# Kernel optimization log

Hardware: AMD Instinct MI355X
Metric: run time of the kernel (lower is better)

The kernel has to match this reference:

```python
import jax, jax.numpy as jnp
import numpy as np
import math

SAMPLING_FACTOR = 5


def setup_inputs() -> dict:
    key = jax.random.key(0)
    kq, kk, kv, ki = jax.random.split(key, 4)
    B, L_Q, L_K, d = 8, 4096, 4096, 64
    # U_part = min(5 * L_Q * ceil(log1p(L_K)), L_K) = 4096 for these sizes
    U_part = min(SAMPLING_FACTOR * L_Q * math.ceil(math.log1p(L_K)), L_K)
    q = jax.random.normal(kq, (B, L_Q, d), dtype=jnp.float32)
    K = jax.random.normal(kk, (B, L_K, d), dtype=jnp.float32)
    V = jax.random.normal(kv, (B, L_K, d), dtype=jnp.float32)
    index_sample = jax.random.randint(ki, (U_part,), 0, L_K)  # random key sample (torch.randint)
    return {"q": q, "K": K, "V": V, "index_sample": index_sample}


def reference(q, K, V, index_sample):
    B, L_Q, d = q.shape
    L_K = K.shape[1]
    log_L_Q = math.ceil(math.log1p(L_Q))
    u = min(SAMPLING_FACTOR * log_L_Q, L_Q)  # number of selected queries (45 here)

    # Random key sampling (indices shared across batch)
    K_sample = K[:, index_sample, :]                       # [B, U_part, d]
    # Q @ K_sample^T
    Q_K_sample = jnp.einsum('bqd,bud->bqu', q, K_sample)   # [B, L_Q, U_part]
    # Sparsity measure M = max - sum/L_K
    M = Q_K_sample.max(axis=-1) - Q_K_sample.sum(axis=-1) / L_K  # [B, L_Q]
    # Source uses topk(..., largest=False): pick queries with SMALLEST M (kept faithfully)
    _, M_top = jax.lax.top_k(-M, u)                        # [B, u]
    # Gather the selected queries
    Q_reduce = jnp.take_along_axis(q, M_top[:, :, None], axis=1)  # [B, u, d]
    # Full attention over all keys for the selected queries
    attn_scores = jnp.einsum('bud,bkd->buk', Q_reduce, K) / math.sqrt(d)  # [B, u, L_K]
    attn_probs = jax.nn.softmax(attn_scores, axis=-1)
    attn_output = jnp.einsum('buk,bkd->bud', attn_probs, V)  # [B, u, d]
    return attn_output, attn_scores
```

## Files before the change

### kernel.cpp

```cpp
#include <hip/hip_runtime.h>
#include <hip/hip_bf16.h>
#include <math.h>

#define BB 8
#define LQ 4096
#define LK 4096
#define DD 64
#define UU 45
#define CCAP 256
#define CUMTHR 96
#define ECH 32
#define PCH 32
#define MCG 4

typedef __bf16 bf16x8 __attribute__((ext_vector_type(8)));
typedef unsigned short ushort8 __attribute__((ext_vector_type(8)));
typedef float f32x4 __attribute__((ext_vector_type(4)));

__device__ inline unsigned short f2bf(float x) {
    unsigned u = __builtin_bit_cast(unsigned, x);
    return (unsigned short)((u + 0x7FFF + ((u >> 16) & 1)) >> 16);
}

__device__ inline void gl_lds16(const void* g, void* l) {
    __builtin_amdgcn_global_load_lds(
        (const __attribute__((address_space(1))) unsigned int*)g,
        (__attribute__((address_space(3))) unsigned int*)l, 16, 0, 0);
}

__global__ __launch_bounds__(256) void k_gatherK(const float* __restrict__ K,
                                                 const int* __restrict__ idx,
                                                 int Upart,
                                                 unsigned short* __restrict__ Kg,
                                                 double* __restrict__ part) {
    int b = blockIdx.y;
    int chunk = blockIdx.x;
    int u0 = chunk * 256;
    int t = threadIdx.x;
    int pt = t & 7;

    double acc[8] = {0,0,0,0,0,0,0,0};
    #pragma unroll
    for (int i = 0; i < 8; ++i) {
        int lin = i * 256 + t;
        int u = u0 + (lin >> 3);
        if (u < Upart) {
            int kr = idx[u];
            const float* src = &K[((size_t)b * LK + kr) * DD + pt * 8];
            float4 v0 = *(const float4*)src;
            float4 v1 = *(const float4*)(src + 4);
            ushort8 pk;
            pk[0]=f2bf(v0.x); pk[1]=f2bf(v0.y); pk[2]=f2bf(v0.z); pk[3]=f2bf(v0.w);
            pk[4]=f2bf(v1.x); pk[5]=f2bf(v1.y); pk[6]=f2bf(v1.z); pk[7]=f2bf(v1.w);
            *(ushort8*)&Kg[((size_t)b * 4096 + u) * 64 + pt * 8] = pk;
            acc[0] += (double)v0.x; acc[1] += (double)v0.y;
            acc[2] += (double)v0.z; acc[3] += (double)v0.w;
            acc[4] += (double)v1.x; acc[5] += (double)v1.y;
            acc[6] += (double)v1.z; acc[7] += (double)v1.w;
        }
    }
    __shared__ double sred[32][64];
    int rg = t >> 3;
    #pragma unroll
    for (int j = 0; j < 8; ++j) sred[rg][pt * 8 + j] = acc[j];
    __syncthreads();
    if (t < 64) {
        double s = 0.0;
        #pragma unroll
        for (int r = 0; r < 32; ++r) s += sred[r][t];
        part[((size_t)(b * 16 + chunk)) * 64 + t] = s;
    }
}

__global__ __launch_bounds__(256) void k_mfmaM(const float* __restrict__ Q,
                                               const unsigned short* __restrict__ Kg,
                                               float* __restrict__ maxpart) {
    int bx = blockIdx.x, cg = blockIdx.y, b = blockIdx.z;
    int t = threadIdx.x;
    int lane = t & 63, w = t >> 6;
    int row0 = bx * 256;

    __shared__ unsigned short Qs[256 * 64];
    __shared__ unsigned short Ks[2][128 * 64];

    for (int i = 0; i < 8; ++i) {
        int u = i * 256 + t;
        int r = u >> 3, s = u & 7;
        int c = s ^ (r & 7);
        const float* src = &Q[((size_t)b * LQ + row0 + r) * DD + c * 8];
        float4 v0 = *(const float4*)src;
        float4 v1 = *(const float4*)(src + 4);
        ushort8 pk;
        pk[0]=f2bf(v0.x); pk[1]=f2bf(v0.y); pk[2]=f2bf(v0.z); pk[3]=f2bf(v0.w);
        pk[4]=f2bf(v1.x); pk[5]=f2bf(v1.y); pk[6]=f2bf(v1.z); pk[7]=f2bf(v1.w);
        *(ushort8*)&Qs[r * 64 + s * 8] = pk;
    }

    int krl = lane >> 3;
    int kc8 = (lane & 7) ^ (krl & 7);
    const unsigned short* kgb = Kg + ((size_t)b * 4096 + cg * 1024) * 64;

    #define STAGE_K(buf, tile)                                                  \
        {                                                                       \
            _Pragma("unroll")                                                   \
            for (int i_ = 0; i_ < 4; ++i_) {                                    \
                int seg_ = w * 4 + i_;                                          \
                const unsigned short* g_ =                                      \
                    kgb + ((size_t)((tile) * 128 + seg_ * 8 + krl)) * 64 + kc8 * 8; \
                gl_lds16(g_, &Ks[buf][seg_ * 512]);                             \
            }                                                                   \
        }

    STAGE_K(0, 0)
    __syncthreads();

    bf16x8 afr[4][2];
    #pragma unroll
    for (int rf = 0; rf < 4; ++rf)
        #pragma unroll
        for (int kh = 0; kh < 2; ++kh) {
            int r = w * 64 + rf * 16 + (lane & 15);
            int slot = (kh * 4 + (lane >> 4)) ^ (r & 7);
            afr[rf][kh] = __builtin_bit_cast(bf16x8, *(const ushort8*)&Qs[r * 64 + slot * 8]);
        }

    float rowmax[4][4];
    #pragma unroll
    for (int rf = 0; rf < 4; ++rf)
        #pragma unroll
        for (int g = 0; g < 4; ++g) rowmax[rf][g] = -INFINITY;

    for (int tile = 0; tile < 8; ++tile) {
        int cur = tile & 1;
        if (tile < 7) STAGE_K(cur ^ 1, tile + 1)

        #pragma unroll
        for (int cf = 0; cf < 8; ++cf) {
            f32x4 acc[4];
            #pragma unroll
            for (int rf = 0; rf < 4; ++rf) acc[rf] = (f32x4){0.f, 0.f, 0.f, 0.f};
            #pragma unroll
            for (int kh = 0; kh < 2; ++kh) {
                int ccol = cf * 16 + (lane & 15);
                int slot = (kh * 4 + (lane >> 4)) ^ (ccol & 7);
                bf16x8 bfr = __builtin_bit_cast(bf16x8, *(const ushort8*)&Ks[cur][ccol * 64 + slot * 8]);
                #pragma unroll
                for (int rf = 0; rf < 4; ++rf)
                    acc[rf] = __builtin_amdgcn_mfma_f32_16x16x32_bf16(afr[rf][kh], bfr, acc[rf], 0, 0, 0);
            }
            #pragma unroll
            for (int rf = 0; rf < 4; ++rf)
                #pragma unroll
                for (int g = 0; g < 4; ++g)
                    rowmax[rf][g] = fmaxf(rowmax[rf][g], acc[rf][g]);
        }
        __syncthreads();
    }

    #pragma unroll
    for (int rf = 0; rf < 4; ++rf)
        #pragma unroll
        for (int g = 0; g < 4; ++g) {
            float m = rowmax[rf][g];
            m = fmaxf(m, __shfl_xor(m, 1));
            m = fmaxf(m, __shfl_xor(m, 2));
            m = fmaxf(m, __shfl_xor(m, 4));
            m = fmaxf(m, __shfl_xor(m, 8));
            if ((lane & 15) == 0) {
                int row = row0 + w * 64 + rf * 16 + (lane >> 4) * 4 + g;
                maxpart[((size_t)(b * MCG + cg)) * LQ + row] = m;
            }
        }
}

__global__ __launch_bounds__(256) void k_meanmerge(const float* __restrict__ Q,
                                                   const double* __restrict__ part,
                                                   int nch,
                                                   const float* __restrict__ maxpart,
                                                   double* __restrict__ mt,
                                                   float* __restrict__ Map) {
    int b = blockIdx.y;
    int t = threadIdx.x;
    int r = blockIdx.x * 256 + t;
    __shared__ double sK[64];
    if (t < 64) {
        double s = 0.0;
        for (int ch = 0; ch < nch; ++ch)
            s += part[((size_t)(b * 16 + ch)) * 64 + t];
        sK[t] = s;
    }
    __syncthreads();
    const float* qr = &Q[((size_t)b * LQ + r) * DD];
    double a0 = 0, a1 = 0, a2 = 0, a3 = 0;
    #pragma unroll
    for (int d = 0; d < 64; d += 4) {
        a0 += (double)qr[d + 0] * sK[d + 0];
        a1 += (double)qr[d + 1] * sK[d + 1];
        a2 += (double)qr[d + 2] * sK[d + 2];
        a3 += (double)qr[d + 3] * sK[d + 3];
    }
    double m = ((a0 + a1) + (a2 + a3)) / (double)LK;
    mt[(size_t)b * LQ + r] = m;
    float mx = fmaxf(fmaxf(maxpart[((size_t)(b * MCG + 0)) * LQ + r],
                           maxpart[((size_t)(b * MCG + 1)) * LQ + r]),
                     fmaxf(maxpart[((size_t)(b * MCG + 2)) * LQ + r],
                           maxpart[((size_t)(b * MCG + 3)) * LQ + r]));
    Map[(size_t)b * LQ + r] = mx - (float)m;
}

__global__ __launch_bounds__(256) void k_select(const float* __restrict__ Map,
                                                int* __restrict__ cand,
                                                int* __restrict__ cand_count) {
    int b = blockIdx.x;
    int t = threadIdx.x;
    __shared__ float mv[LQ];
    __shared__ int hist[1024];
    __shared__ int seg[256];
    __shared__ float wmin[4], wmax[4];
    __shared__ float s_min, s_max;
    __shared__ int s_bstar, s_cnt;

    float lmin = INFINITY, lmax = -INFINITY;
    for (int i = t; i < LQ; i += 256) {
        float v = Map[(size_t)b * LQ + i];
        mv[i] = v;
        lmin = fminf(lmin, v);
        lmax = fmaxf(lmax, v);
    }
    #pragma unroll
    for (int m = 1; m < 64; m <<= 1) {
        lmin = fminf(lmin, __shfl_xor(lmin, m));
        lmax = fmaxf(lmax, __shfl_xor(lmax, m));
    }
    int wid = t >> 6;
    if ((t & 63) == 0) { wmin[wid] = lmin; wmax[wid] = lmax; }
    for (int i = t; i < 1024; i += 256) hist[i] = 0;
    __syncthreads();
    if (t == 0) {
        s_min = fminf(fminf(wmin[0], wmin[1]), fminf(wmin[2], wmin[3]));
        s_max = fmaxf(fmaxf(wmax[0], wmax[1]), fmaxf(wmax[2], wmax[3]));
        s_cnt = 0;
        s_bstar = 1023;
    }
    __syncthreads();
    float vmin = s_min;
    float w = (s_max - vmin) * (1.0f / 1024.0f);
    if (w <= 0.f) w = 1e-30f;
    float inv = 1.0f / w;
    for (int i = t; i < LQ; i += 256) {
        int bin = (int)((mv[i] - vmin) * inv);
        bin = min(max(bin, 0), 1023);
        atomicAdd(&hist[bin], 1);
    }
    __syncthreads();
    int h0 = hist[t * 4 + 0], h1 = hist[t * 4 + 1];
    int h2 = hist[t * 4 + 2], h3 = hist[t * 4 + 3];
    seg[t] = h0 + h1 + h2 + h3;
    __syncthreads();
    for (int off = 1; off < 256; off <<= 1) {
        int v = seg[t];
        int add = (t >= off) ? seg[t - off] : 0;
        __syncthreads();
        seg[t] = v + add;
        __syncthreads();
    }
    {
        int prev = (t == 0) ? 0 : seg[t - 1];
        if (seg[t] >= CUMTHR && prev < CUMTHR) {
            int cum = prev, bs = t * 4 + 3;
            if (cum + h0 >= CUMTHR) bs = t * 4;
            else if (cum + h0 + h1 >= CUMTHR) bs = t * 4 + 1;
            else if (cum + h0 + h1 + h2 >= CUMTHR) bs = t * 4 + 2;
            s_bstar = bs;
        }
    }
    __syncthreads();
    int bstar = s_bstar;
    for (int i = t; i < LQ; i += 256) {
        int bin = (int)((mv[i] - vmin) * inv);
        bin = min(max(bin, 0), 1023);
        if (bin <= bstar) {
            int p = atomicAdd(&s_cnt, 1);
            if (p < CCAP) cand[b * CCAP + p] = i;
        }
    }
    __syncthreads();
    if (t == 0) cand_count[b] = min(s_cnt, CCAP);
}

__global__ __launch_bounds__(256, 1) void k_exact(const float* __restrict__ Q,
                                                  const float* __restrict__ K,
                                                  const int* __restrict__ idx,
                                                  const int* __restrict__ cand,
                                                  const int* __restrict__ cand_count,
                                                  float* __restrict__ exactpart) {
    int kc = blockIdx.x;
    int b  = blockIdx.y;
    int t = threadIdx.x;
    int lane = t & 63, w = t >> 6;
    __shared__ float Ks[128 * 64];
    __shared__ float wmx[4][CCAP];

    #pragma unroll
    for (int p = 0; p < 8; ++p) {
        int row = p * 16 + (t >> 4);
        int c4 = t & 15;
        int kr = idx[kc * 128 + row];
        *(float4*)&Ks[row * 64 + c4 * 4] =
            *(const float4*)&K[((size_t)b * LK + kr) * DD + c4 * 4];
    }

    int count = cand_count[b];
    int npass = (count + 127) >> 7;
    __syncthreads();

    for (int pass = 0; pass < npass; ++pass) {
        int s0 = pass * 128 + lane;
        int s1 = s0 + 64;
        float4 q0[16], q1[16];
        {
            float4 z = {0.f, 0.f, 0.f, 0.f};
            if (s0 < count) {
                const float4* qp = (const float4*)&Q[((size_t)b * LQ + cand[b * CCAP + s0]) * DD];
                #pragma unroll
                for (int i = 0; i < 16; ++i) q0[i] = qp[i];
            } else {
                #pragma unroll
                for (int i = 0; i < 16; ++i) q0[i] = z;
            }
            if (s1 < count) {
                const float4* qp = (const float4*)&Q[((size_t)b * LQ + cand[b * CCAP + s1]) * DD];
                #pragma unroll
                for (int i = 0; i < 16; ++i) q1[i] = qp[i];
            } else {
                #pragma unroll
                for (int i = 0; i < 16; ++i) q1[i] = z;
            }
        }

        float m0 = -INFINITY, m1 = -INFINITY;
        int kbeg = w * 32;
        for (int k = kbeg; k < kbeg + 32; ++k) {
            const float4* kr4 = (const float4*)&Ks[k * 64];
            float a0=0.f,a1=0.f,a2=0.f,a3=0.f;
            float c0=0.f,c1=0.f,c2=0.f,c3=0.f;
            #pragma unroll
            for (int i = 0; i < 16; i += 4) {
                float4 kv0 = kr4[i+0], kv1 = kr4[i+1], kv2 = kr4[i+2], kv3 = kr4[i+3];
                a0 = fmaf(q0[i+0].x, kv0.x, a0); a0 = fmaf(q0[i+0].y, kv0.y, a0);
                a0 = fmaf(q0[i+0].z, kv0.z, a0); a0 = fmaf(q0[i+0].w, kv0.w, a0);
                a1 = fmaf(q0[i+1].x, kv1.x, a1); a1 = fmaf(q0[i+1].y, kv1.y, a1);
                a1 = fmaf(q0[i+1].z, kv1.z, a1); a1 = fmaf(q0[i+1].w, kv1.w, a1);
                a2 = fmaf(q0[i+2].x, kv2.x, a2); a2 = fmaf(q0[i+2].y, kv2.y, a2);
                a2 = fmaf(q0[i+2].z, kv2.z, a2); a2 = fmaf(q0[i+2].w, kv2.w, a2);
                a3 = fmaf(q0[i+3].x, kv3.x, a3); a3 = fmaf(q0[i+3].y, kv3.y, a3);
                a3 = fmaf(q0[i+3].z, kv3.z, a3); a3 = fmaf(q0[i+3].w, kv3.w, a3);
                c0 = fmaf(q1[i+0].x, kv0.x, c0); c0 = fmaf(q1[i+0].y, kv0.y, c0);
                c0 = fmaf(q1[i+0].z, kv0.z, c0); c0 = fmaf(q1[i+0].w, kv0.w, c0);
                c1 = fmaf(q1[i+1].x, kv1.x, c1); c1 = fmaf(q1[i+1].y, kv1.y, c1);
                c1 = fmaf(q1[i+1].z, kv1.z, c1); c1 = fmaf(q1[i+1].w, kv1.w, c1);
                c2 = fmaf(q1[i+2].x, kv2.x, c2); c2 = fmaf(q1[i+2].y, kv2.y, c2);
                c2 = fmaf(q1[i+2].z, kv2.z, c2); c2 = fmaf(q1[i+2].w, kv2.w, c2);
                c3 = fmaf(q1[i+3].x, kv3.x, c3); c3 = fmaf(q1[i+3].y, kv3.y, c3);
                c3 = fmaf(q1[i+3].z, kv3.z, c3); c3 = fmaf(q1[i+3].w, kv3.w, c3);
            }
            m0 = fmaxf(m0, (a0 + a1) + (a2 + a3));
            m1 = fmaxf(m1, (c0 + c1) + (c2 + c3));
        }
        wmx[w][s0] = m0;
        if (s1 < CCAP) wmx[w][s1] = m1;
    }
    __syncthreads();

    if (t < count) {
        float m = fmaxf(fmaxf(wmx[0][t], wmx[1][t]), fmaxf(wmx[2][t], wmx[3][t]));
        exactpart[((size_t)(b * CCAP + t)) * ECH + kc] = m;
    }
}

__global__ __launch_bounds__(64) void k_final45(const float* __restrict__ exactpart,
                                                const double* __restrict__ mt,
                                                const int* __restrict__ cand,
                                                const int* __restrict__ cand_count,
                                                int* __restrict__ Mtop) {
    int b = blockIdx.x;
    int l = threadIdx.x;
    int count = cand_count[b];
    float val[4];
    int oid[4];
    #pragma unroll
    for (int j = 0; j < 4; ++j) {
        int slot = l + j * 64;
        if (slot < count) {
            const float* ep = &exactpart[((size_t)(b * CCAP + slot)) * ECH];
            float m = ep[0];
            #pragma unroll
            for (int k = 1; k < ECH; ++k) m = fmaxf(m, ep[k]);
            int r = cand[b * CCAP + slot];
            val[j] = m - (float)mt[(size_t)b * LQ + r];
            oid[j] = r;
        } else { val[j] = INFINITY; oid[j] = 0x7FFFFFFF; }
    }
    for (int it = 0; it < UU; ++it) {
        float bv = val[0]; int bi = oid[0], bj = 0;
        #pragma unroll
        for (int j = 1; j < 4; ++j)
            if (val[j] < bv || (val[j] == bv && oid[j] < bi)) { bv = val[j]; bi = oid[j]; bj = j; }
        float rv = bv; int ri = bi;
        #pragma unroll
        for (int m = 1; m < 64; m <<= 1) {
            float ov = __shfl_xor(rv, m);
            int oi = __shfl_xor(ri, m);
            if (ov < rv || (ov == rv && oi < ri)) { rv = ov; ri = oi; }
        }
        if (l == 0) Mtop[b * UU + it] = ri;
        if (rv == bv && ri == bi) val[bj] = INFINITY;
    }
}

__global__ __launch_bounds__(256) void k_spv(const float* __restrict__ Q,
                                             const float* __restrict__ K,
                                             const float* __restrict__ V,
                                             const int* __restrict__ Mtop,
                                             float* __restrict__ scores,
                                             float2* __restrict__ stats,
                                             float* __restrict__ partial) {
    int ch = blockIdx.x, b = blockIdx.y;
    int t = threadIdx.x;
    int lane = t & 63, w = t >> 6;
    int k0 = ch * 128;

    __shared__ float Qs[48][64];
    __shared__ float Vs[128 * 64];
    __shared__ float Ps[48][128];
    __shared__ float2 st[48];

    for (int i = t; i < 48 * 64; i += 256) {
        int r = i >> 6, dd = i & 63;
        Qs[r][dd] = (r < UU) ? Q[((size_t)b * LQ + Mtop[b * UU + r]) * DD + dd] : 0.f;
    }
    for (int p = 0; p < 8; ++p) {
        int lin = p * 1024 + t * 4;
        *(float4*)&Vs[lin] = *(const float4*)&V[((size_t)b * LK + k0) * DD + lin];
    }
    __syncthreads();

    {
        int key = t & 127;
        int rh = t >> 7;
        int r0 = rh * 23;
        int r1 = rh ? UU : 23;
        const float* Krow = &K[((size_t)(b * LK + k0 + key)) * DD];
        float4 kv[16];
        #pragma unroll
        for (int i = 0; i < 16; ++i) kv[i] = ((const float4*)Krow)[i];
        for (int r = r0; r < r1; ++r) {
            const float4* qr = (const float4*)&Qs[r][0];
            float d0 = 0.f, d1 = 0.f, d2 = 0.f, d3 = 0.f;
            #pragma unroll
            for (int i = 0; i < 16; i += 4) {
                float4 q0 = qr[i+0], q1 = qr[i+1], q2 = qr[i+2], q3 = qr[i+3];
                d0 = fmaf(q0.x, kv[i+0].x, d0); d0 = fmaf(q0.y, kv[i+0].y, d0);
                d0 = fmaf(q0.z, kv[i+0].z, d0); d0 = fmaf(q0.w, kv[i+0].w, d0);
                d1 = fmaf(q1.x, kv[i+1].x, d1); d1 = fmaf(q1.y, kv[i+1].y, d1);
                d1 = fmaf(q1.z, kv[i+1].z, d1); d1 = fmaf(q1.w, kv[i+1].w, d1);
                d2 = fmaf(q2.x, kv[i+2].x, d2); d2 = fmaf(q2.y, kv[i+2].y, d2);
                d2 = fmaf(q2.z, kv[i+2].z, d2); d2 = fmaf(q2.w, kv[i+2].w, d2);
                d3 = fmaf(q3.x, kv[i+3].x, d3); d3 = fmaf(q3.y, kv[i+3].y, d3);
                d3 = fmaf(q3.z, kv[i+3].z, d3); d3 = fmaf(q3.w, kv[i+3].w, d3);
            }
            float sc = ((d0 + d1) + (d2 + d3)) * 0.125f;
            Ps[r][key] = sc;
            scores[((size_t)(b * UU + r)) * LK + k0 + key] = sc;
        }
    }
    __syncthreads();

    for (int r = w; r < 48; r += 4) {
        if (r < UU) {
            float v0 = Ps[r][lane], v1 = Ps[r][lane + 64];
            float m = fmaxf(v0, v1);
            #pragma unroll
            for (int o = 32; o; o >>= 1) m = fmaxf(m, __shfl_xor(m, o));
            float e0 = __expf(v0 - m), e1 = __expf(v1 - m);
            float s = e0 + e1;
            #pragma unroll
            for (int o = 32; o; o >>= 1) s += __shfl_xor(s, o);
            Ps[r][lane] = e0; Ps[r][lane + 64] = e1;
            if (lane == 0) st[r] = make_float2(m, s);
        } else {
            Ps[r][lane] = 0.f; Ps[r][lane + 64] = 0.f;
        }
    }
    __syncthreads();

    {
        int d = t & 63, rg = t >> 6;
        float acc[12];
        #pragma unroll
        for (int i = 0; i < 12; ++i) acc[i] = 0.f;
        for (int k = 0; k < 128; ++k) {
            float vv = Vs[k * 64 + d];
            #pragma unroll
            for (int i = 0; i < 12; ++i)
                acc[i] += Ps[rg * 12 + i][k] * vv;
        }
        #pragma unroll
        for (int i = 0; i < 12; ++i) {
            int r = rg * 12 + i;
            if (r < UU)
                partial[(((size_t)(b * PCH + ch)) * UU + r) * 64 + d] = acc[i];
        }
    }
    if (t < UU) stats[((size_t)(b * PCH + ch)) * UU + t] = st[t];
}

__global__ __launch_bounds__(256) void k_combine(const float* __restrict__ partial,
                                                 const float2* __restrict__ stats,
                                                 float* __restrict__ out) {
    int b = blockIdx.x;
    int t = threadIdx.x;
    __shared__ float wgt[UU][PCH];
    if (t < UU) {
        float mx[PCH], sm[PCH];
        #pragma unroll
        for (int c = 0; c < PCH; ++c) {
            float2 v = stats[((size_t)(b * PCH + c)) * UU + t];
            mx[c] = v.x; sm[c] = v.y;
        }
        float m = mx[0];
        #pragma unroll
        for (int c = 1; c < PCH; ++c) m = fmaxf(m, mx[c]);
        float S = 0.f;
        #pragma unroll
        for (int c = 0; c < PCH; ++c) {
            float e = __expf(mx[c] - m);
            wgt[t][c] = e;
            S += sm[c] * e;
        }
        float inv = 1.0f / S;
        #pragma unroll
        for (int c = 0; c < PCH; ++c) wgt[t][c] *= inv;
    }
    __syncthreads();
    for (int o = t; o < UU * 64; o += 256) {
        int r = o >> 6, d = o & 63;
        float s = 0.f;
        #pragma unroll 8
        for (int c = 0; c < PCH; ++c)
            s += partial[(((size_t)(b * PCH + c)) * UU + r) * 64 + d] * wgt[r][c];
        out[((size_t)(b * UU + r)) * 64 + d] = s;
    }
}

extern "C" void kernel_launch(void* const* d_in, const int* in_sizes, int n_in,
                              void* d_out, int out_size, void* d_ws, size_t ws_size,
                              hipStream_t stream) {
    const float* q   = (const float*)d_in[0];
    const float* K   = (const float*)d_in[1];
    const float* V   = (const float*)d_in[2];
    const int*   idx = (const int*)d_in[3];
    int Upart = in_sizes[3];
    int nch = (Upart + 255) / 256;

    char* ws = (char*)d_ws;
    size_t off = 0;
    unsigned short* Kg = (unsigned short*)(ws + off); off += (size_t)BB * 4096 * 64 * 2;
    float*  maxpart   = (float*)(ws + off);  off += (size_t)BB * MCG * LQ * 4;
    double* mt        = (double*)(ws + off); off += (size_t)BB * LQ * 8;
    float*  Map       = (float*)(ws + off);  off += (size_t)BB * LQ * 4;
    int*    cand      = (int*)(ws + off);    off += (size_t)BB * CCAP * 4;
    int*    cand_cnt  = (int*)(ws + off);    off += 256;
    int*    Mtop      = (int*)(ws + off);    off += 2048;
    float2* stats     = (float2*)(ws + off); off += (size_t)BB * PCH * UU * 8 + 256;
    float*  partial   = (float*)(ws + off);  off += (size_t)BB * PCH * UU * 64 * 4;
    double* sumKpart  = (double*)partial;
    float*  exactpart = (float*)partial;

    float* out_attn   = (float*)d_out;
    float* out_scores = out_attn + BB * UU * 64;

    k_gatherK  <<<dim3(nch, BB), 256, 0, stream>>>(K, idx, Upart, Kg, sumKpart);
    k_mfmaM    <<<dim3(LQ / 256, MCG, BB), 256, 0, stream>>>(q, Kg, maxpart);
    k_meanmerge<<<dim3(LQ / 256, BB), 256, 0, stream>>>(q, sumKpart, nch, maxpart, mt, Map);
    k_select   <<<dim3(BB), 256, 0, stream>>>(Map, cand, cand_cnt);
    k_exact    <<<dim3(ECH, BB), 256, 0, stream>>>(q, K, idx, cand, cand_cnt, exactpart);
    k_final45  <<<dim3(BB), 64, 0, stream>>>(exactpart, mt, cand, cand_cnt, Mtop);
    k_spv      <<<dim3(PCH, BB), 256, 0, stream>>>(q, K, V, Mtop, out_scores, stats, partial);
    k_combine  <<<dim3(BB), 256, 0, stream>>>(partial, stats, out_attn);
}
```

Baseline: 155.9 us.

## Shrink mfmaM LDS by aliasing Q and K buffers; widen gather and select

Q is staged into LDS and loaded into register fragments first, after which the same 32 KB buffer is reused as the double-buffered K tiles. This halves k_mfmaM's LDS footprint so more blocks can be resident per CU. The K gather now uses 128-row chunks, giving twice as many blocks, and k_select runs with 1024 threads per block to spread its per-batch histogram work. The aliasing adds an extra barrier, and the wider select block leaves most threads idle during the 256-wide scan.

```diff
diff --git a/kernel.cpp b/kernel.cpp
--- a/kernel.cpp
+++ b/kernel.cpp
@@ -12,6 +12,7 @@
 #define ECH 32
 #define PCH 32
 #define MCG 4
+#define GCH 32
 
 typedef __bf16 bf16x8 __attribute__((ext_vector_type(8)));
 typedef unsigned short ushort8 __attribute__((ext_vector_type(8)));
@@ -35,13 +36,13 @@
                                                  double* __restrict__ part) {
     int b = blockIdx.y;
     int chunk = blockIdx.x;
-    int u0 = chunk * 256;
+    int u0 = chunk * 128;
     int t = threadIdx.x;
     int pt = t & 7;
 
     double acc[8] = {0,0,0,0,0,0,0,0};
     #pragma unroll
-    for (int i = 0; i < 8; ++i) {
+    for (int i = 0; i < 4; ++i) {
         int lin = i * 256 + t;
         int u = u0 + (lin >> 3);
         if (u < Upart) {
@@ -68,7 +69,7 @@
         double s = 0.0;
         #pragma unroll
         for (int r = 0; r < 32; ++r) s += sred[r][t];
-        part[((size_t)(b * 16 + chunk)) * 64 + t] = s;
+        part[((size_t)(b * GCH + chunk)) * 64 + t] = s;
     }
 }
 
@@ -80,8 +81,7 @@
     int lane = t & 63, w = t >> 6;
     int row0 = bx * 256;
 
-    __shared__ unsigned short Qs[256 * 64];
-    __shared__ unsigned short Ks[2][128 * 64];
+    __shared__ unsigned short smem[16384];
 
     for (int i = 0; i < 8; ++i) {
         int u = i * 256 + t;
@@ -93,8 +93,20 @@
         ushort8 pk;
         pk[0]=f2bf(v0.x); pk[1]=f2bf(v0.y); pk[2]=f2bf(v0.z); pk[3]=f2bf(v0.w);
         pk[4]=f2bf(v1.x); pk[5]=f2bf(v1.y); pk[6]=f2bf(v1.z); pk[7]=f2bf(v1.w);
-        *(ushort8*)&Qs[r * 64 + s * 8] = pk;
-    }
+        *(ushort8*)&smem[r * 64 + s * 8] = pk;
+    }
+    __syncthreads();
+
+    bf16x8 afr[4][2];
+    #pragma unroll
+    for (int rf = 0; rf < 4; ++rf)
+        #pragma unroll
+        for (int kh = 0; kh < 2; ++kh) {
+            int r = w * 64 + rf * 16 + (lane & 15);
+            int slot = (kh * 4 + (lane >> 4)) ^ (r & 7);
+            afr[rf][kh] = __builtin_bit_cast(bf16x8, *(const ushort8*)&smem[r * 64 + slot * 8]);
+        }
+    __syncthreads();
 
     int krl = lane >> 3;
     int kc8 = (lane & 7) ^ (krl & 7);
@@ -107,22 +119,12 @@
                 int seg_ = w * 4 + i_;                                          \
                 const unsigned short* g_ =                                      \
                     kgb + ((size_t)((tile) * 128 + seg_ * 8 + krl)) * 64 + kc8 * 8; \
-                gl_lds16(g_, &Ks[buf][seg_ * 512]);                             \
+                gl_lds16(g_, &smem[(buf) * 8192 + seg_ * 512]);                 \
             }                                                                   \
         }
 
     STAGE_K(0, 0)
     __syncthreads();
-
-    bf16x8 afr[4][2];
-    #pragma unroll
-    for (int rf = 0; rf < 4; ++rf)
-        #pragma unroll
-        for (int kh = 0; kh < 2; ++kh) {
-            int r = w * 64 + rf * 16 + (lane & 15);
-            int slot = (kh * 4 + (lane >> 4)) ^ (r & 7);
-            afr[rf][kh] = __builtin_bit_cast(bf16x8, *(const ushort8*)&Qs[r * 64 + slot * 8]);
-        }
 
     float rowmax[4][4];
     #pragma unroll
@@ -143,7 +145,8 @@
             for (int kh = 0; kh < 2; ++kh) {
                 int ccol = cf * 16 + (lane & 15);
                 int slot = (kh * 4 + (lane >> 4)) ^ (ccol & 7);
-                bf16x8 bfr = __builtin_bit_cast(bf16x8, *(const ushort8*)&Ks[cur][ccol * 64 + slot * 8]);
+                bf16x8 bfr = __builtin_bit_cast(bf16x8,
+                    *(const ushort8*)&smem[cur * 8192 + ccol * 64 + slot * 8]);
                 #pragma unroll
                 for (int rf = 0; rf < 4; ++rf)
                     acc[rf] = __builtin_amdgcn_mfma_f32_16x16x32_bf16(afr[rf][kh], bfr, acc[rf], 0, 0, 0);
@@ -186,7 +189,7 @@
     if (t < 64) {
         double s = 0.0;
         for (int ch = 0; ch < nch; ++ch)
-            s += part[((size_t)(b * 16 + ch)) * 64 + t];
+            s += part[((size_t)(b * GCH + ch)) * 64 + t];
         sK[t] = s;
     }
     __syncthreads();
@@ -208,20 +211,20 @@
     Map[(size_t)b * LQ + r] = mx - (float)m;
 }
 
-__global__ __launch_bounds__(256) void k_select(const float* __restrict__ Map,
-                                                int* __restrict__ cand,
-                                                int* __restrict__ cand_count) {
+__global__ __launch_bounds__(1024) void k_select(const float* __restrict__ Map,
+                                                 int* __restrict__ cand,
+                                                 int* __restrict__ cand_count) {
     int b = blockIdx.x;
     int t = threadIdx.x;
     __shared__ float mv[LQ];
     __shared__ int hist[1024];
     __shared__ int seg[256];
-    __shared__ float wmin[4], wmax[4];
+    __shared__ float wmin[16], wmax[16];
     __shared__ float s_min, s_max;
     __shared__ int s_bstar, s_cnt;
 
     float lmin = INFINITY, lmax = -INFINITY;
-    for (int i = t; i < LQ; i += 256) {
+    for (int i = t; i < LQ; i += 1024) {
         float v = Map[(size_t)b * LQ + i];
         mv[i] = v;
         lmin = fminf(lmin, v);
@@ -234,11 +237,13 @@
     }
     int wid = t >> 6;
     if ((t & 63) == 0) { wmin[wid] = lmin; wmax[wid] = lmax; }
-    for (int i = t; i < 1024; i += 256) hist[i] = 0;
+    if (t < 1024) hist[t] = 0;
     __syncthreads();
     if (t == 0) {
-        s_min = fminf(fminf(wmin[0], wmin[1]), fminf(wmin[2], wmin[3]));
-        s_max = fmaxf(fmaxf(wmax[0], wmax[1]), fmaxf(wmax[2], wmax[3]));
+        float mn = wmin[0], mx = wmax[0];
+        #pragma unroll
+        for (int i = 1; i < 16; ++i) { mn = fminf(mn, wmin[i]); mx = fmaxf(mx, wmax[i]); }
+        s_min = mn; s_max = mx;
         s_cnt = 0;
         s_bstar = 1023;
     }
@@ -247,24 +252,27 @@
     float w = (s_max - vmin) * (1.0f / 1024.0f);
     if (w <= 0.f) w = 1e-30f;
     float inv = 1.0f / w;
-    for (int i = t; i < LQ; i += 256) {
+    for (int i = t; i < LQ; i += 1024) {
         int bin = (int)((mv[i] - vmin) * inv);
         bin = min(max(bin, 0), 1023);
         atomicAdd(&hist[bin], 1);
     }
     __syncthreads();
-    int h0 = hist[t * 4 + 0], h1 = hist[t * 4 + 1];
-    int h2 = hist[t * 4 + 2], h3 = hist[t * 4 + 3];
-    seg[t] = h0 + h1 + h2 + h3;
+    int h0 = 0, h1 = 0, h2 = 0, h3 = 0;
+    if (t < 256) {
+        h0 = hist[t * 4 + 0]; h1 = hist[t * 4 + 1];
+        h2 = hist[t * 4 + 2]; h3 = hist[t * 4 + 3];
+        seg[t] = h0 + h1 + h2 + h3;
+    }
     __syncthreads();
     for (int off = 1; off < 256; off <<= 1) {
-        int v = seg[t];
-        int add = (t >= off) ? seg[t - off] : 0;
+        int v = 0, add = 0;
+        if (t < 256) { v = seg[t]; add = (t >= off) ? seg[t - off] : 0; }
         __syncthreads();
-        seg[t] = v + add;
+        if (t < 256) seg[t] = v + add;
         __syncthreads();
     }
-    {
+    if (t < 256) {
         int prev = (t == 0) ? 0 : seg[t - 1];
         if (seg[t] >= CUMTHR && prev < CUMTHR) {
             int cum = prev, bs = t * 4 + 3;
@@ -276,7 +284,7 @@
     }
     __syncthreads();
     int bstar = s_bstar;
-    for (int i = t; i < LQ; i += 256) {
+    for (int i = t; i < LQ; i += 1024) {
         int bin = (int)((mv[i] - vmin) * inv);
         bin = min(max(bin, 0), 1023);
         if (bin <= bstar) {
@@ -561,7 +569,7 @@
     const float* V   = (const float*)d_in[2];
     const int*   idx = (const int*)d_in[3];
     int Upart = in_sizes[3];
-    int nch = (Upart + 255) / 256;
+    int nch = (Upart + 127) / 128;
 
     char* ws = (char*)d_ws;
     size_t off = 0;
@@ -583,7 +591,7 @@
     k_gatherK  <<<dim3(nch, BB), 256, 0, stream>>>(K, idx, Upart, Kg, sumKpart);
     k_mfmaM    <<<dim3(LQ / 256, MCG, BB), 256, 0, stream>>>(q, Kg, maxpart);
     k_meanmerge<<<dim3(LQ / 256, BB), 256, 0, stream>>>(q, sumKpart, nch, maxpart, mt, Map);
-    k_select   <<<dim3(BB), 256, 0, stream>>>(Map, cand, cand_cnt);
+    k_select   <<<dim3(BB), 1024, 0, stream>>>(Map, cand, cand_cnt);
     k_exact    <<<dim3(ECH, BB), 256, 0, stream>>>(q, K, idx, cand, cand_cnt, exactpart);
     k_final45  <<<dim3(BB), 64, 0, stream>>>(exactpart, mt, cand, cand_cnt, Mtop);
     k_spv      <<<dim3(PCH, BB), 256, 0, stream>>>(q, K, V, Mtop, out_scores, stats, partial);
```

Result: faster. 151.3 us (-3.0%).
